# Performance work log

Measured on AMD Instinct MI355X. Metric: run time of the kernel, lower is better.

## Reference

```python
import jax, jax.numpy as jnp
import numpy as np
import math
from jax import lax

STRIDES = (8.0, 16.0, 32.0)
ANCHORS = (
    ((6.1, 8.1), (20.6, 12.6), (11.2, 23.7)),
    ((36.2, 26.8), (25.9, 57.2), (57.8, 47.9)),
    ((122.1, 78.3), (73.7, 143.8), (236.1, 213.1)),
)
NUM_CLASSES = 80
L = NUM_CLASSES + 5
NA = 3
SCORE_T = 0.1
NMS_T = 0.6
DETECTIONS = 100
TOPK = 1000          # static cap on post-threshold candidates per image
IMG = 640            # batched image H=W; also max_size used for class offsets


def setup_inputs() -> dict:
    key = jax.random.key(0)
    ks = jax.random.split(key, 8)
    N = 8
    chans = (128, 256, 512)
    hw = (80, 40, 20)
    inp = {}
    for i, (c, s) in enumerate(zip(chans, hw)):
        inp[f"f{i}"] = jax.random.normal(ks[i], (N, c, s, s), jnp.float32)
        inp[f"w{i}"] = jax.random.normal(ks[3 + i], (NA * L, c), jnp.float32) * 0.02
        b = np.zeros((NA, L), np.float32)
        b[:, 4] += math.log(8 / (416 / STRIDES[i]) ** 2)   # Predictor bias init
        b[:, 5:] += math.log(0.6 / (NUM_CLASSES - 0.99))
        inp[f"b{i}"] = jnp.asarray(b.reshape(-1))
    inp["scale_factors"] = jnp.ones((N,), jnp.float32)
    return inp


def _decode_level(f, w, b, stride, anchors):
    # f: [N,Cin,H,W]; w: [NA*L,Cin]; 1x1 conv == channel GEMM
    N, _, H, W = f.shape
    p = jnp.einsum('nchw,oc->nhwo', f, w) + b
    p = jax.nn.sigmoid(p.reshape(N, H, W, NA, L))
    gx, gy = jnp.meshgrid(jnp.arange(W, dtype=f.dtype), jnp.arange(H, dtype=f.dtype), indexing='xy')
    grid = jnp.stack((gx, gy), axis=-1)                       # [H,W,2] (x,y)
    xy = (2 * p[..., :2] - 0.5 + grid[None, :, :, None, :]) * stride
    wh = 4 * p[..., 2:4] ** 2 * anchors[None, None, None, :, :]
    box = jnp.concatenate((xy, wh), axis=-1).reshape(N, -1, 4)
    obj = p[..., 4].reshape(N, -1)
    cls = p[..., 5:].reshape(N, -1, NUM_CLASSES)
    return box, obj, cls


def _cxcywh2xyxy(b):
    cx, cy, w, h = b[..., 0], b[..., 1], b[..., 2], b[..., 3]
    return jnp.stack((cx - w / 2, cy - h / 2, cx + w / 2, cy + h / 2), axis=-1)


def _iou_one_many(b, boxes):
    lt = jnp.maximum(b[:2], boxes[:, :2])
    rb = jnp.minimum(b[2:], boxes[:, 2:])
    wh = jnp.clip(rb - lt, 0)
    inter = wh[:, 0] * wh[:, 1]
    area_b = (b[2] - b[0]) * (b[3] - b[1])
    areas = (boxes[:, 2] - boxes[:, 0]) * (boxes[:, 3] - boxes[:, 1])
    return inter / (area_b + areas - inter + 1e-7)


def _nms_fixed(boxes, scores):
    # greedy NMS, fixed DETECTIONS iterations; boxes already class-offset
    def step(valid, _):
        s = jnp.where(valid, scores, -jnp.inf)
        i = jnp.argmax(s)
        ok = s[i] > 0.0
        ious = _iou_one_many(boxes[i], boxes)
        nv = valid & (ious <= NMS_T)
        nv = nv.at[i].set(False)
        valid = jnp.where(ok, nv, valid)
        return valid, (jnp.where(ok, i, -1), ok)

    valid0 = scores > SCORE_T
    _, (idx, ok) = lax.scan(step, valid0, None, length=DETECTIONS)
    return idx, ok


def _per_image(boxes, obj, cls, sf):
    scores = obj[:, None] * cls                               # [A,C]
    mask = (obj[:, None] > SCORE_T) & (scores > SCORE_T)
    scores = jnp.where(mask, scores, -1.0)
    topv, topi = lax.top_k(scores.reshape(-1), TOPK)
    anchor = topi // NUM_CLASSES
    label = topi % NUM_CLASSES
    cb = boxes[anchor]
    cb = jnp.clip(cb, 0.0, float(IMG))                        # image_shapes = (IMG, IMG)
    off = cb + (label * IMG).astype(cb.dtype)[:, None]        # batched_nms class offset
    idx, ok = _nms_fixed(off, topv)
    gi = jnp.clip(idx, 0)
    okf = ok.astype(cb.dtype)
    out_box = cb[gi] / sf * okf[:, None]
    out_score = topv[gi] * okf
    out_label = label[gi].astype(cb.dtype) * okf
    return jnp.concatenate((out_box, out_score[:, None], out_label[:, None]), axis=1)  # [DET,6]


def reference(f0, f1, f2, w0, b0, w1, b1, w2, b2, scale_factors):
    feats = (f0, f1, f2)
    ws = (w0, w1, w2)
    bs = (b0, b1, b2)
    boxes, objs, clss = [], [], []
    for i in range(3):
        a = jnp.asarray(ANCHORS[i], dtype=f0.dtype)
        bx, ob, cl = _decode_level(feats[i], ws[i], bs[i], STRIDES[i], a)
        boxes.append(bx)
        objs.append(ob)
        clss.append(cl)
    boxes = _cxcywh2xyxy(jnp.concatenate(boxes, axis=1))      # [N, 25200, 4]
    obj = jnp.concatenate(objs, axis=1)                       # [N, 25200]
    cls = jnp.concatenate(clss, axis=1)                       # [N, 25200, 80]
    return jax.vmap(_per_image)(boxes, obj, cls, scale_factors)  # [N, DET, 6]
```

## Files before the change

kernel.cpp:

```cpp
#include <hip/hip_runtime.h>
#include <math.h>


#define IMG_F 640.0f

#define WT_F     0
#define N_WT     344064
#define WT_L0    0
#define WT_L1    49152
#define WT_L2    147456
#define CNTB_F   344064
#define IMGCNT_F 344768
#define NSLOT    64
#define CANDB_F  344776
#define IMGBUF_F (CANDB_F + 700 * NSLOT * 2)
#define CAP2     2048

#define LOGIT_T (-2.1972245773362196f)

__constant__ float d_anch[3][3][2] = {
  {{6.1f,8.1f},{20.6f,12.6f},{11.2f,23.7f}},
  {{36.2f,26.8f},{25.9f,57.2f},{57.8f,47.9f}},
  {{122.1f,78.3f},{73.7f,143.8f},{236.1f,213.1f}},
};
__constant__ float d_stridec[3] = {8.f,16.f,32.f};

__global__ __launch_bounds__(256) void kb_obj(
    const float* __restrict__ f0, const float* __restrict__ f1,
    const float* __restrict__ f2,
    const float* __restrict__ w0, const float* __restrict__ w1,
    const float* __restrict__ w2,
    const float* __restrict__ b0, const float* __restrict__ b1,
    const float* __restrict__ b2, float* __restrict__ ws) {
  __shared__ float red[3104];
  __shared__ int lcnt;
  int b = blockIdx.x, t = threadIdx.x;
  if (t == 0) lcnt = 0;
  if (b == 0 && t < 8) ((int*)ws)[IMGCNT_F + t] = 0;
  for (int i = b * 256 + t; i < N_WT; i += 700 * 256) {
    int C, i2; const float* w;
    if (i < WT_L1)      { C = 128; i2 = i;         w = w0; }
    else if (i < WT_L2) { C = 256; i2 = i - WT_L1; w = w1; }
    else                { C = 512; i2 = i - WT_L2; w = w2; }
    int a = i2 / (C * 128);
    int r = i2 - a * (C * 128);
    int c = r >> 7, l = r & 127;
    ws[WT_F + i] = (l < 85) ? w[(size_t)(a * 85 + l) * C + c] : 0.f;
  }
  int level, Q, lq, S, bq0, C, HW;
  const float *f, *w, *bb;
  if (b < 400)      { level = 0; Q = 32; lq = 5; S = 8;  bq0 = b * 32;         C = 128; HW = 6400; f = f0; w = w0; bb = b0; }
  else if (b < 600) { level = 1; Q = 16; lq = 4; S = 16; bq0 = (b - 400) * 16; C = 256; HW = 1600; f = f1; w = w1; bb = b1; }
  else              { level = 2; Q = 8;  lq = 3; S = 32; bq0 = (b - 600) * 8;  C = 512; HW = 400;  f = f2; w = w2; bb = b2; }
  int q = t & (Q - 1), sl = t >> lq;
  int qpi = HW >> 2;
  int gq = bq0 + q;
  int n = gq / qpi;
  int sq = (gq - n * qpi) << 2;
  int kbase = sl * 16;
  const float* fp = f + ((size_t)(n * C + kbase)) * HW + sq;
  const float* wp = w + 4 * C + kbase;
  float acc[3][4] = {{0.f,0.f,0.f,0.f},{0.f,0.f,0.f,0.f},{0.f,0.f,0.f,0.f}};
  #pragma unroll
  for (int c = 0; c < 16; ++c) {
    float4 v = *(const float4*)(fp + (size_t)c * HW);
    float wa0 = wp[c];
    float wa1 = wp[85 * C + c];
    float wa2 = wp[170 * C + c];
    acc[0][0] = fmaf(v.x, wa0, acc[0][0]); acc[0][1] = fmaf(v.y, wa0, acc[0][1]);
    acc[0][2] = fmaf(v.z, wa0, acc[0][2]); acc[0][3] = fmaf(v.w, wa0, acc[0][3]);
    acc[1][0] = fmaf(v.x, wa1, acc[1][0]); acc[1][1] = fmaf(v.y, wa1, acc[1][1]);
    acc[1][2] = fmaf(v.z, wa1, acc[1][2]); acc[1][3] = fmaf(v.w, wa1, acc[1][3]);
    acc[2][0] = fmaf(v.x, wa2, acc[2][0]); acc[2][1] = fmaf(v.y, wa2, acc[2][1]);
    acc[2][2] = fmaf(v.z, wa2, acc[2][2]); acc[2][3] = fmaf(v.w, wa2, acc[2][3]);
  }
  int stride = Q * 12 + 1;
  int base = sl * stride + q * 12;
  #pragma unroll
  for (int a = 0; a < 3; ++a)
    #pragma unroll
    for (int p = 0; p < 4; ++p)
      red[base + a * 4 + p] = acc[a][p];
  __syncthreads();
  for (int r = t; r < Q * 12; r += 256) {
    int qq = r / 12, ap = r - qq * 12;
    int a = ap >> 2, p = ap & 3;
    float sum = 0.f;
    for (int s2 = 0; s2 < S; ++s2) sum += red[s2 * stride + qq * 12 + ap];
    float logit = sum + bb[a * 85 + 4];
    if (logit > LOGIT_T) {
      float obj = 1.f / (1.f + expf(-logit));
      int gq2 = bq0 + qq;
      int n2 = gq2 / qpi;
      int s = ((gq2 - n2 * qpi) << 2) + p;
      int idx = atomicAdd(&lcnt, 1);
      if (idx < NSLOT) {
        int* cd = (int*)ws + CANDB_F + (b * NSLOT + idx) * 2;
        cd[0] = (n2 << 24) | (level << 20) | (a << 16) | s;
        ((float*)cd)[1] = obj;
      }
    }
  }
  __syncthreads();
  if (t == 0) ((int*)ws)[CNTB_F + b] = min(lcnt, NSLOT);
}

template<int C, int HW, int Wd>
__device__ __forceinline__ void kc_block(
    int level, int n, int a, int s, float obj,
    const float* __restrict__ f, const float* __restrict__ wTl,
    const float* __restrict__ bb, float* __restrict__ ws,
    float* __restrict__ fc, float* __restrict__ partial,
    float* __restrict__ sig, int tid) {
  for (int i = tid; i < C; i += 256)
    fc[i] = f[((size_t)(n * C + i)) * HW + s];
  __syncthreads();
  int sl = tid >> 6, lane = tid & 63;
  const float* wA = wTl + (size_t)a * C * 128;
  constexpr int CQ = C / 4;
  const float* wp = wA + (size_t)(sl * CQ) * 128;
  const float* fq = fc + sl * CQ;
  float2 acc = {0.f, 0.f};
  #pragma unroll 8
  for (int c = 0; c < CQ; ++c) {
    float fv = fq[c];
    float2 wv = *(const float2*)(wp + (size_t)c * 128 + 2 * lane);
    acc.x = fmaf(fv, wv.x, acc.x);
    acc.y = fmaf(fv, wv.y, acc.y);
  }
  *(float2*)(partial + sl * 128 + 2 * lane) = acc;
  __syncthreads();
  if (tid < 85) {
    float sum = partial[tid] + partial[128 + tid] + partial[256 + tid] + partial[384 + tid];
    float logit = sum + bb[a * 85 + tid];
    sig[tid] = 1.f / (1.f + expf(-logit));
  }
  __syncthreads();
  float p0 = sig[0], p1 = sig[1], p2 = sig[2], p3 = sig[3];
  int gx = s % Wd, gy = s / Wd;
  float st = d_stridec[level];
  float cx = (2.f * p0 - 0.5f + (float)gx) * st;
  float cy = (2.f * p1 - 0.5f + (float)gy) * st;
  float bw = 4.f * p2 * p2 * d_anch[level][a][0];
  float bh = 4.f * p3 * p3 * d_anch[level][a][1];
  float x1 = fminf(fmaxf(cx - bw * 0.5f, 0.f), IMG_F);
  float y1 = fminf(fmaxf(cy - bh * 0.5f, 0.f), IMG_F);
  float x2 = fminf(fmaxf(cx + bw * 0.5f, 0.f), IMG_F);
  float y2 = fminf(fmaxf(cy + bh * 0.5f, 0.f), IMG_F);
  if (tid >= 5 && tid < 85) {
    float sc = obj * sig[tid];
    if (sc > 0.1f) {
      int p = atomicAdd((int*)ws + IMGCNT_F + n, 1);
      if (p < CAP2) {
        float* dst = ws + IMGBUF_F + ((size_t)(n * CAP2 + p)) * 6;
        dst[0] = x1; dst[1] = y1; dst[2] = x2; dst[3] = y2;
        dst[4] = sc; dst[5] = (float)(tid - 5);
      }
    }
  }
  __syncthreads();
}

__global__ __launch_bounds__(256) void kc_score(
    const float* __restrict__ f0, const float* __restrict__ f1,
    const float* __restrict__ f2,
    const float* __restrict__ b0, const float* __restrict__ b1,
    const float* __restrict__ b2, float* __restrict__ ws) {
  __shared__ float fc[512];
  __shared__ float partial[512];
  __shared__ float sig[85];
  int tid = threadIdx.x;
  int reg = blockIdx.x >> 3, ci0 = blockIdx.x & 7;
  int cnt = min(((int*)ws)[CNTB_F + reg], NSLOT);
  for (int ci = ci0; ci < cnt; ci += 8) {
    int* cd = (int*)ws + CANDB_F + (reg * NSLOT + ci) * 2;
    int code = cd[0]; float obj = ((float*)cd)[1];
    int n = code >> 24, level = (code >> 20) & 15, a = (code >> 16) & 3, s = code & 0xFFFF;
    if (level == 0)
      kc_block<128, 6400, 80>(0, n, a, s, obj, f0, ws + WT_F + WT_L0, b0, ws, fc, partial, sig, tid);
    else if (level == 1)
      kc_block<256, 1600, 40>(1, n, a, s, obj, f1, ws + WT_F + WT_L1, b1, ws, fc, partial, sig, tid);
    else
      kc_block<512, 400, 20>(2, n, a, s, obj, f2, ws + WT_F + WT_L2, b2, ws, fc, partial, sig, tid);
  }
}

__global__ __launch_bounds__(256) void kd_nms(
    const float* __restrict__ ws, float* __restrict__ out,
    const float* __restrict__ sfp) {
  __shared__ float bx1[CAP2], by1[CAP2], bx2[CAP2], by2[CAP2], bsc[CAP2], blb[CAP2];
  __shared__ int bval[CAP2];
  __shared__ float rs[256];
  __shared__ int ri[256];
  int n = blockIdx.x, tid = threadIdx.x;
  int cnt = min(((const int*)ws)[IMGCNT_F + n], CAP2);
  for (int i = tid; i < cnt; i += 256) {
    const float* src = ws + IMGBUF_F + ((size_t)(n * CAP2 + i)) * 6;
    bx1[i] = src[0]; by1[i] = src[1]; bx2[i] = src[2]; by2[i] = src[3];
    bsc[i] = src[4]; blb[i] = src[5]; bval[i] = 1;
  }
  __syncthreads();
  float sf = sfp[n];
  for (int it = 0; it < 100; ++it) {
    float best = -1.f; int bi = -1;
    for (int i = tid; i < cnt; i += 256)
      if (bval[i] && bsc[i] > best) { best = bsc[i]; bi = i; }
    rs[tid] = best; ri[tid] = bi;
    __syncthreads();
    for (int off = 128; off > 0; off >>= 1) {
      if (tid < off && rs[tid + off] > rs[tid]) { rs[tid] = rs[tid + off]; ri[tid] = ri[tid + off]; }
      __syncthreads();
    }
    int wi = ri[0]; float wsc = rs[0];
    if (wi < 0) {
      for (int r2 = it * 6 + tid; r2 < 600; r2 += 256)
        out[(size_t)n * 600 + r2] = 0.f;
      break;
    }
    if (tid == 0) {
      float* o = out + (size_t)(n * 100 + it) * 6;
      o[0] = bx1[wi] / sf; o[1] = by1[wi] / sf;
      o[2] = bx2[wi] / sf; o[3] = by2[wi] / sf;
      o[4] = wsc;          o[5] = blb[wi];
    }
    float ofw = blb[wi] * IMG_F;
    float wx1 = bx1[wi] + ofw, wy1 = by1[wi] + ofw;
    float wx2 = bx2[wi] + ofw, wy2 = by2[wi] + ofw;
    float wa = (wx2 - wx1) * (wy2 - wy1);
    for (int i = tid; i < cnt; i += 256) {
      if (bval[i]) {
        float o2 = blb[i] * IMG_F;
        float x1 = bx1[i] + o2, y1 = by1[i] + o2, x2 = bx2[i] + o2, y2 = by2[i] + o2;
        float iw = fmaxf(fminf(wx2, x2) - fmaxf(wx1, x1), 0.f);
        float ih = fmaxf(fminf(wy2, y2) - fmaxf(wy1, y1), 0.f);
        float inter = iw * ih;
        float area = (x2 - x1) * (y2 - y1);
        float iou = inter / (wa + area - inter + 1e-7f);
        if (iou > 0.6f) bval[i] = 0;
      }
    }
    if (tid == 0) bval[wi] = 0;
    __syncthreads();
  }
}

extern "C" void kernel_launch(void* const* d_in, const int* in_sizes, int n_in,
                              void* d_out, int out_size, void* d_ws, size_t ws_size,
                              hipStream_t stream) {
  const float* f0 = (const float*)d_in[0];
  const float* w0 = (const float*)d_in[1];
  const float* b0 = (const float*)d_in[2];
  const float* f1 = (const float*)d_in[3];
  const float* w1 = (const float*)d_in[4];
  const float* b1 = (const float*)d_in[5];
  const float* f2 = (const float*)d_in[6];
  const float* w2 = (const float*)d_in[7];
  const float* b2 = (const float*)d_in[8];
  const float* sf = (const float*)d_in[9];
  float* out = (float*)d_out;
  float* ws  = (float*)d_ws;

  kb_obj  <<<700,    256, 0, stream>>>(f0, f1, f2, w0, w1, w2, b0, b1, b2, ws);
  kc_score<<<700 * 8, 256, 0, stream>>>(f0, f1, f2, b0, b1, b2, ws);
  kd_nms  <<<8,      256, 0, stream>>>(ws, out, sf);
}
```

Before: 126.5 us.

## Fuse NMS into scoring kernel via last-block election and widen GEMV slices

Removes the separate NMS launch by having the last finishing block of the scoring kernel, found through an atomic done-counter and threadfence, run NMS for all 8 images in sequence. NMS now reads boxes from global memory instead of staging them in shared memory, and tracks suppression by setting scores to -1. The per-candidate GEMV is also regrouped into 8 channel slices of 32 lanes using float4 loads. The cost is that NMS runs serially over 8 images on a single block instead of 8 blocks in parallel, which adds tail latency.

```diff
diff --git a/kernel.cpp b/kernel.cpp
--- a/kernel.cpp
+++ b/kernel.cpp
@@ -11,8 +11,9 @@
 #define WT_L2    147456
 #define CNTB_F   344064
 #define IMGCNT_F 344768
+#define DONE_F   344776
 #define NSLOT    64
-#define CANDB_F  344776
+#define CANDB_F  344780
 #define IMGBUF_F (CANDB_F + 700 * NSLOT * 2)
 #define CAP2     2048
 
@@ -36,7 +37,7 @@
   __shared__ int lcnt;
   int b = blockIdx.x, t = threadIdx.x;
   if (t == 0) lcnt = 0;
-  if (b == 0 && t < 8) ((int*)ws)[IMGCNT_F + t] = 0;
+  if (b == 0 && t < 9) ((int*)ws)[IMGCNT_F + t] = 0;
   for (int i = b * 256 + t; i < N_WT; i += 700 * 256) {
     int C, i2; const float* w;
     if (i < WT_L1)      { C = 128; i2 = i;         w = w0; }
@@ -115,23 +116,27 @@
   for (int i = tid; i < C; i += 256)
     fc[i] = f[((size_t)(n * C + i)) * HW + s];
   __syncthreads();
-  int sl = tid >> 6, lane = tid & 63;
+  int slice = tid >> 5, lane5 = tid & 31;
   const float* wA = wTl + (size_t)a * C * 128;
-  constexpr int CQ = C / 4;
-  const float* wp = wA + (size_t)(sl * CQ) * 128;
-  const float* fq = fc + sl * CQ;
-  float2 acc = {0.f, 0.f};
-  #pragma unroll 8
-  for (int c = 0; c < CQ; ++c) {
+  constexpr int CS = C / 8;
+  const float* wp = wA + (size_t)(slice * CS) * 128 + 4 * lane5;
+  const float* fq = fc + slice * CS;
+  float4 acc = {0.f, 0.f, 0.f, 0.f};
+  #pragma unroll 16
+  for (int c = 0; c < CS; ++c) {
     float fv = fq[c];
-    float2 wv = *(const float2*)(wp + (size_t)c * 128 + 2 * lane);
+    float4 wv = *(const float4*)(wp + (size_t)c * 128);
     acc.x = fmaf(fv, wv.x, acc.x);
     acc.y = fmaf(fv, wv.y, acc.y);
-  }
-  *(float2*)(partial + sl * 128 + 2 * lane) = acc;
+    acc.z = fmaf(fv, wv.z, acc.z);
+    acc.w = fmaf(fv, wv.w, acc.w);
+  }
+  *(float4*)(partial + slice * 128 + 4 * lane5) = acc;
   __syncthreads();
   if (tid < 85) {
-    float sum = partial[tid] + partial[128 + tid] + partial[256 + tid] + partial[384 + tid];
+    float sum = 0.f;
+    #pragma unroll
+    for (int k = 0; k < 8; ++k) sum += partial[k * 128 + tid];
     float logit = sum + bb[a * 85 + tid];
     sig[tid] = 1.f / (1.f + expf(-logit));
   }
@@ -161,16 +166,19 @@
   __syncthreads();
 }
 
-__global__ __launch_bounds__(256) void kc_score(
+__global__ __launch_bounds__(256) void kc_nms(
     const float* __restrict__ f0, const float* __restrict__ f1,
     const float* __restrict__ f2,
     const float* __restrict__ b0, const float* __restrict__ b1,
-    const float* __restrict__ b2, float* __restrict__ ws) {
-  __shared__ float fc[512];
-  __shared__ float partial[512];
-  __shared__ float sig[85];
+    const float* __restrict__ b2, float* __restrict__ ws,
+    float* __restrict__ out, const float* __restrict__ sfp) {
+  __shared__ float smem[2576];
+  __shared__ int isLast;
   int tid = threadIdx.x;
   int reg = blockIdx.x >> 3, ci0 = blockIdx.x & 7;
+  float* fc = smem;
+  float* partial = smem + 512;
+  float* sig = smem + 1536;
   int cnt = min(((int*)ws)[CNTB_F + reg], NSLOT);
   for (int ci = ci0; ci < cnt; ci += 8) {
     int* cd = (int*)ws + CANDB_F + (reg * NSLOT + ci) * 2;
@@ -183,63 +191,69 @@
     else
       kc_block<512, 400, 20>(2, n, a, s, obj, f2, ws + WT_F + WT_L2, b2, ws, fc, partial, sig, tid);
   }
-}
-
-__global__ __launch_bounds__(256) void kd_nms(
-    const float* __restrict__ ws, float* __restrict__ out,
-    const float* __restrict__ sfp) {
-  __shared__ float bx1[CAP2], by1[CAP2], bx2[CAP2], by2[CAP2], bsc[CAP2], blb[CAP2];
-  __shared__ int bval[CAP2];
-  __shared__ float rs[256];
-  __shared__ int ri[256];
-  int n = blockIdx.x, tid = threadIdx.x;
-  int cnt = min(((const int*)ws)[IMGCNT_F + n], CAP2);
-  for (int i = tid; i < cnt; i += 256) {
-    const float* src = ws + IMGBUF_F + ((size_t)(n * CAP2 + i)) * 6;
-    bx1[i] = src[0]; by1[i] = src[1]; bx2[i] = src[2]; by2[i] = src[3];
-    bsc[i] = src[4]; blb[i] = src[5]; bval[i] = 1;
-  }
-  __syncthreads();
-  float sf = sfp[n];
-  for (int it = 0; it < 100; ++it) {
-    float best = -1.f; int bi = -1;
-    for (int i = tid; i < cnt; i += 256)
-      if (bval[i] && bsc[i] > best) { best = bsc[i]; bi = i; }
-    rs[tid] = best; ri[tid] = bi;
+  __syncthreads();
+  if (tid == 0) {
+    __threadfence();
+    int old = atomicAdd((int*)ws + DONE_F, 1);
+    isLast = (old == (int)gridDim.x - 1);
+  }
+  __syncthreads();
+  if (!isLast) return;
+  __threadfence();
+  float* bscv = smem;
+  float* rs   = smem + 2048;
+  int*   ri   = (int*)(smem + 2304);
+  float* bc   = smem + 2560;
+  for (int n = 0; n < 8; ++n) {
+    float sf = sfp[n];
+    int bcnt = min(((int*)ws)[IMGCNT_F + n], CAP2);
+    const float* ibuf = ws + IMGBUF_F + (size_t)n * CAP2 * 6;
+    for (int i = tid; i < bcnt; i += 256) bscv[i] = ibuf[(size_t)i * 6 + 4];
     __syncthreads();
-    for (int off = 128; off > 0; off >>= 1) {
-      if (tid < off && rs[tid + off] > rs[tid]) { rs[tid] = rs[tid + off]; ri[tid] = ri[tid + off]; }
+    for (int it = 0; it < 100; ++it) {
+      float best = -1.f; int bi = -1;
+      for (int i = tid; i < bcnt; i += 256)
+        if (bscv[i] > best) { best = bscv[i]; bi = i; }
+      rs[tid] = best; ri[tid] = bi;
+      __syncthreads();
+      for (int off = 128; off > 0; off >>= 1) {
+        if (tid < off && rs[tid + off] > rs[tid]) { rs[tid] = rs[tid + off]; ri[tid] = ri[tid + off]; }
+        __syncthreads();
+      }
+      int wi = ri[0]; float wsc = rs[0];
+      if (wi < 0 || wsc <= 0.f) {
+        for (int r2 = it * 6 + tid; r2 < 600; r2 += 256)
+          out[(size_t)n * 600 + r2] = 0.f;
+        break;
+      }
+      if (tid == 0) {
+        const float* src = ibuf + (size_t)wi * 6;
+        float x1 = src[0], y1 = src[1], x2 = src[2], y2 = src[3], lb = src[5];
+        float* o = out + (size_t)(n * 100 + it) * 6;
+        o[0] = x1 / sf; o[1] = y1 / sf; o[2] = x2 / sf; o[3] = y2 / sf;
+        o[4] = wsc;     o[5] = lb;
+        float ofw = lb * IMG_F;
+        bc[0] = x1 + ofw; bc[1] = y1 + ofw; bc[2] = x2 + ofw; bc[3] = y2 + ofw;
+        bc[4] = (x2 - x1) * (y2 - y1);
+        bscv[wi] = -1.f;
+      }
+      __syncthreads();
+      float wx1 = bc[0], wy1 = bc[1], wx2 = bc[2], wy2 = bc[3], wa = bc[4];
+      for (int i = tid; i < bcnt; i += 256) {
+        if (bscv[i] > 0.f) {
+          const float* s2 = ibuf + (size_t)i * 6;
+          float o2 = s2[5] * IMG_F;
+          float x1 = s2[0] + o2, y1 = s2[1] + o2, x2 = s2[2] + o2, y2 = s2[3] + o2;
+          float iw = fmaxf(fminf(wx2, x2) - fmaxf(wx1, x1), 0.f);
+          float ih = fmaxf(fminf(wy2, y2) - fmaxf(wy1, y1), 0.f);
+          float inter = iw * ih;
+          float area = (x2 - x1) * (y2 - y1);
+          float iou = inter / (wa + area - inter + 1e-7f);
+          if (iou > 0.6f) bscv[i] = -1.f;
+        }
+      }
       __syncthreads();
     }
-    int wi = ri[0]; float wsc = rs[0];
-    if (wi < 0) {
-      for (int r2 = it * 6 + tid; r2 < 600; r2 += 256)
-        out[(size_t)n * 600 + r2] = 0.f;
-      break;
-    }
-    if (tid == 0) {
-      float* o = out + (size_t)(n * 100 + it) * 6;
-      o[0] = bx1[wi] / sf; o[1] = by1[wi] / sf;
-      o[2] = bx2[wi] / sf; o[3] = by2[wi] / sf;
-      o[4] = wsc;          o[5] = blb[wi];
-    }
-    float ofw = blb[wi] * IMG_F;
-    float wx1 = bx1[wi] + ofw, wy1 = by1[wi] + ofw;
-    float wx2 = bx2[wi] + ofw, wy2 = by2[wi] + ofw;
-    float wa = (wx2 - wx1) * (wy2 - wy1);
-    for (int i = tid; i < cnt; i += 256) {
-      if (bval[i]) {
-        float o2 = blb[i] * IMG_F;
-        float x1 = bx1[i] + o2, y1 = by1[i] + o2, x2 = bx2[i] + o2, y2 = by2[i] + o2;
-        float iw = fmaxf(fminf(wx2, x2) - fmaxf(wx1, x1), 0.f);
-        float ih = fmaxf(fminf(wy2, y2) - fmaxf(wy1, y1), 0.f);
-        float inter = iw * ih;
-        float area = (x2 - x1) * (y2 - y1);
-        float iou = inter / (wa + area - inter + 1e-7f);
-        if (iou > 0.6f) bval[i] = 0;
-      }
-    }
-    if (tid == 0) bval[wi] = 0;
     __syncthreads();
   }
 }
@@ -260,7 +274,6 @@
   float* out = (float*)d_out;
   float* ws  = (float*)d_ws;
 
-  kb_obj  <<<700,    256, 0, stream>>>(f0, f1, f2, w0, w1, w2, b0, b1, b2, ws);
-  kc_score<<<700 * 8, 256, 0, stream>>>(f0, f1, f2, b0, b1, b2, ws);
-  kd_nms  <<<8,      256, 0, stream>>>(ws, out, sf);
-}
+  kb_obj <<<700,     256, 0, stream>>>(f0, f1, f2, w0, w1, w2, b0, b1, b2, ws);
+  kc_nms <<<700 * 8, 256, 0, stream>>>(f0, f1, f2, b0, b1, b2, ws, out, sf);
+}
```

Measured after the change: 212.3 us. +67.9%, slower.
